# Performance work log

Measured on AMD Instinct MI355X. Metric: run time of the kernel, lower is better.

The kernel has to match this reference:

```python
import jax, jax.numpy as jnp
import numpy as np

HEADS = 16
MAX_SEQ_LEN = 1024
ALPHA = 1.0


def setup_inputs() -> dict:
    key = jax.random.key(0)
    ks = jax.random.split(key, 16)
    b, n, dim = 2, 1024, 1024
    s = 0.02
    x = jax.random.normal(ks[0], (b, n, dim), jnp.float32)
    Wq = jax.random.normal(ks[1], (dim, dim), jnp.float32) * s
    Wk = jax.random.normal(ks[2], (dim, dim), jnp.float32) * s
    Wv = jax.random.normal(ks[3], (dim, dim), jnp.float32) * s
    Wo = jax.random.normal(ks[4], (dim, dim), jnp.float32) * s
    E_idx = jax.random.normal(ks[5], (MAX_SEQ_LEN, HEADS), jnp.float32) * s
    # padding_idx=0 rows zero-initialized (as in torch nn.Embedding(padding_idx=0))
    E_bar = (jax.random.normal(ks[6], (17, HEADS), jnp.float32) * s).at[0].set(0.0)
    E_pos = (jax.random.normal(ks[7], (96, HEADS), jnp.float32) * s).at[0].set(0.0)
    E_oct = (jax.random.normal(ks[8], (25, HEADS), jnp.float32) * s).at[0].set(0.0)
    E_semi = (jax.random.normal(ks[9], (13, HEADS), jnp.float32) * s).at[0].set(0.0)
    # structure matrices: raw values in [0, table_size-2]; forward adds +1
    bar = jax.random.randint(ks[10], (b, n, n), 0, 16, dtype=jnp.int32)
    position = jax.random.randint(ks[11], (b, n, n), 0, 95, dtype=jnp.int32)
    octave = jax.random.randint(ks[12], (b, n, n), 0, 24, dtype=jnp.int32)
    semitone = jax.random.randint(ks[13], (b, n, n), 0, 12, dtype=jnp.int32)
    return {"x": x, "Wq": Wq, "Wk": Wk, "Wv": Wv, "Wo": Wo,
            "E_idx": E_idx, "E_bar": E_bar, "E_pos": E_pos,
            "E_oct": E_oct, "E_semi": E_semi,
            "bar": bar, "position": position, "octave": octave, "semitone": semitone}


def reference(x, Wq, Wk, Wv, Wo, E_idx, E_bar, E_pos, E_oct, E_semi,
              bar, position, octave, semitone):
    b, n, dim = x.shape
    h = HEADS
    d = dim // h

    def split_heads(t):  # (b,n,dim) -> (b,h,n,d)
        return t.reshape(b, n, h, d).transpose(0, 2, 1, 3)

    q = split_heads(x @ Wq.T)
    k = split_heads(x @ Wk.T)
    v = split_heads(x @ Wv.T)

    qk = jnp.einsum('bhid,bhjd->bhij', q, k)

    # relative index bias: (1,h,n,n)
    rel_pos = jnp.clip(jnp.arange(n)[:, None] - jnp.arange(n)[None, :], 0, MAX_SEQ_LEN - 1)
    srel = E_idx[rel_pos].transpose(2, 0, 1)[None]

    # structure biases: embedding lookups -> (b,h,n,n)
    s_time = (E_bar[bar + 1] + E_pos[position + 1]).transpose(0, 3, 1, 2)
    s_pitch = (E_oct[octave + 1] + E_semi[semitone + 1]).transpose(0, 3, 1, 2)

    dots = (qk + ALPHA * (srel + s_time + s_pitch)) / jnp.sqrt(jnp.float32(d))

    causal_mask = jnp.triu(jnp.ones((n, n), dtype=bool), k=1)
    mask_value = -jnp.finfo(dots.dtype).max
    dots = jnp.where(causal_mask, mask_value, dots)

    attn = jax.nn.softmax(dots, axis=-1)  # dropout=0 at eval
    out = jnp.einsum('bhij,bhjd->bhid', attn, v)
    out = out.transpose(0, 2, 1, 3).reshape(b, n, dim)
    return out @ Wo.T
```

## Files before the change

kernel.cpp:

```cpp
#include <hip/hip_runtime.h>
#include <cstdint>
#include <math.h>

typedef __attribute__((ext_vector_type(8))) short short8;
typedef __attribute__((ext_vector_type(4))) float f32x4;

#define LOG2E 1.44269504088896340736f

static __device__ __forceinline__ float bf2f(unsigned short u) {
    union { unsigned int i; float f; } v; v.i = ((unsigned int)u) << 16; return v.f;
}
static __device__ __forceinline__ unsigned short f2bf(float f) {
    union { float f; unsigned int i; } v; v.f = f;
    unsigned int r = v.i + 0x7FFF + ((v.i >> 16) & 1);
    return (unsigned short)(r >> 16);
}

__global__ __launch_bounds__(256) void k_prep(
    const float* __restrict__ x, const float* __restrict__ wq,
    const float* __restrict__ wk, const float* __restrict__ wv,
    const float* __restrict__ wo, unsigned short* __restrict__ dstconv,
    const float* __restrict__ Eidx, const float* __restrict__ Ebar,
    const float* __restrict__ Epos, const float* __restrict__ Eoct,
    const float* __restrict__ Esemi,
    const int* __restrict__ barm, const int* __restrict__ posm,
    const int* __restrict__ octm, const int* __restrict__ semim,
    unsigned short* __restrict__ biasg) {
    __shared__ float2 t2[8 * 233];
    __shared__ int    pk[16 * 65];

    if (blockIdx.x >= 1088) {
        long t = (long)(blockIdx.x - 1088) * 256 + threadIdx.x;
        long base = t * 4;
        const long NX = 2097152, NW = 1048576;
        const float* src; long off;
        if (base < NX)            { src = x;  off = base; }
        else if (base < NX + NW)  { src = wq; off = base - NX; }
        else if (base < NX + 2*NW){ src = wk; off = base - NX - NW; }
        else if (base < NX + 3*NW){ src = wv; off = base - NX - 2*NW; }
        else                      { src = wo; off = base - NX - 3*NW; }
        float4 v = *(const float4*)(src + off);
        ushort4 o;
        o.x = f2bf(v.x); o.y = f2bf(v.y); o.z = f2bf(v.z); o.w = f2bf(v.w);
        *(ushort4*)(dstconv + base) = o;
        return;
    }
    int fid = blockIdx.x;
    int b = (fid >= 544) ? 1 : 0;
    int f = fid - b * 544;
    int ti, tj;
    if (f >= 480) { int rr = f - 480; ti = 60 + (rr >> 4); tj = rr & 15; }
    else {
        int g = (int)(0.5f * (sqrtf(1.0f + 2.0f * (float)f) - 1.0f));
        while (2 * (g + 1) * (g + 2) <= f) g++;
        while (2 * g * (g + 1) > f) g--;
        int rr = f - 2 * g * (g + 1);
        int q = rr / (g + 1);
        ti = g * 4 + q;
        tj = rr - q * (g + 1);
    }
    int i0 = ti * 16, j0 = tj * 64;

    int t = threadIdx.x;
    int rel_lo = i0 - j0 - 63; if (rel_lo < 0) rel_lo = 0;

    for (int idx = t; idx < 231 * 8; idx += 256) {
        int s = idx >> 3, h2 = idx & 7;
        float va, vb;
        if (s < 80) {
            int src = rel_lo + s; if (src > 1023) src = 1023;
            va = Eidx[src * 16 + h2]; vb = Eidx[src * 16 + h2 + 8];
        } else if (s < 97)  { va = Ebar[(s - 80) * 16 + h2];  vb = Ebar[(s - 80) * 16 + h2 + 8]; }
        else if (s < 193)   { va = Epos[(s - 97) * 16 + h2];  vb = Epos[(s - 97) * 16 + h2 + 8]; }
        else if (s < 218)   { va = Eoct[(s - 193) * 16 + h2]; vb = Eoct[(s - 193) * 16 + h2 + 8]; }
        else                { va = Esemi[(s - 218) * 16 + h2]; vb = Esemi[(s - 218) * 16 + h2 + 8]; }
        t2[h2 * 233 + s] = make_float2(va, vb);
    }
    #pragma unroll
    for (int cc = 0; cc < 4; cc++) {
        int cell = t + cc * 256;
        int i = i0 + (cell >> 6), j = j0 + (cell & 63);
        long ij = ((long)b << 20) + ((long)i << 10) + j;
        int v = (barm[ij] + 1) | ((posm[ij] + 1) << 5) |
                ((octm[ij] + 1) << 12) | ((semim[ij] + 1) << 17);
        pk[(cell >> 6) * 65 + (cell & 63)] = v;
    }
    __syncthreads();

    int lane = t & 63, q = t & 15, G = (t >> 4) & 3, hq = t >> 6;
    int base_rel = (i0 + q) - j0 - rel_lo;
    const float2* TA = &t2[hq * 233];
    const float2* TB = &t2[(hq + 4) * 233];
    long tbase = ((((long)(b * 16) * 64 + ti) * 16 + tj) << 10) + lane * 16;
    #pragma unroll
    for (int sub = 0; sub < 4; sub++) {
        ushort4 o0, o1, o2, o3;
        #pragma unroll
        for (int rr = 0; rr < 4; rr++) {
            int key = sub * 16 + G * 4 + rr;
            int p = pk[q * 65 + key];
            int sr = base_rel - key; if (sr < 0) sr = 0;
            float2 a0 = TA[sr];
            float2 a1 = TA[80  + (p & 31)];
            float2 a2 = TA[97  + ((p >> 5)  & 127)];
            float2 a3 = TA[193 + ((p >> 12) & 31)];
            float2 a4 = TA[218 + ((p >> 17) & 15)];
            float2 b0 = TB[sr];
            float2 b1 = TB[80  + (p & 31)];
            float2 b2 = TB[97  + ((p >> 5)  & 127)];
            float2 b3 = TB[193 + ((p >> 12) & 31)];
            float2 b4 = TB[218 + ((p >> 17) & 15)];
            float xA = a0.x + a1.x + a2.x + a3.x + a4.x;
            float yA = a0.y + a1.y + a2.y + a3.y + a4.y;
            float xB = b0.x + b1.x + b2.x + b3.x + b4.x;
            float yB = b0.y + b1.y + b2.y + b3.y + b4.y;
            ((unsigned short*)&o0)[rr] = f2bf(xA * 0.125f);
            ((unsigned short*)&o1)[rr] = f2bf(xB * 0.125f);
            ((unsigned short*)&o2)[rr] = f2bf(yA * 0.125f);
            ((unsigned short*)&o3)[rr] = f2bf(yB * 0.125f);
        }
        *(ushort4*)(biasg + tbase + ((long)hq        << 20) + sub * 4) = o0;
        *(ushort4*)(biasg + tbase + ((long)(hq + 4)  << 20) + sub * 4) = o1;
        *(ushort4*)(biasg + tbase + ((long)(hq + 8)  << 20) + sub * 4) = o2;
        *(ushort4*)(biasg + tbase + ((long)(hq + 12) << 20) + sub * 4) = o3;
    }
}

__global__ __launch_bounds__(256) void k_gemm(
    const unsigned short* __restrict__ A,
    const unsigned short* __restrict__ B0, const unsigned short* __restrict__ B1,
    const unsigned short* __restrict__ B2,
    unsigned short* __restrict__ qd, unsigned short* __restrict__ kd,
    unsigned short* __restrict__ vtd, float* __restrict__ outf, int mode) {
    __shared__ unsigned short As[128 * 64];
    __shared__ unsigned short Bs[64 * 64];
    int md = (mode < 0) ? (int)blockIdx.z : mode;
    const unsigned short* B = (md == 1) ? B1 : (md == 2) ? B2 : B0;
    int m0 = blockIdx.x * 128, n0 = blockIdx.y * 64;
    int t = threadIdx.x;
    int w = t >> 6, lane = t & 63, g = lane >> 4, c = lane & 15;
    int wr = w >> 1, wc = w & 1;
    const int K = 1024;
    f32x4 zero = {0.f, 0.f, 0.f, 0.f};
    f32x4 acc[4][2];
    #pragma unroll
    for (int m = 0; m < 4; m++)
        #pragma unroll
        for (int n = 0; n < 2; n++) acc[m][n] = zero;

    int srow = w * 8 + (lane >> 3);
    int scol = (lane & 7) * 8;
    for (int k0 = 0; k0 < K; k0 += 64) {
        __syncthreads();
        #pragma unroll
        for (int qq = 0; qq < 4; qq++) {
            int row = qq * 32 + srow;
            __builtin_amdgcn_global_load_lds(
                (const __attribute__((address_space(1))) unsigned int*)(A + (long)(m0 + row) * K + k0 + scol),
                (__attribute__((address_space(3))) unsigned int*)&As[(qq * 32 + w * 8) * 64],
                16, 0, 0);
        }
        #pragma unroll
        for (int qq = 0; qq < 2; qq++) {
            int row = qq * 32 + srow;
            __builtin_amdgcn_global_load_lds(
                (const __attribute__((address_space(1))) unsigned int*)(B + (long)(n0 + row) * K + k0 + scol),
                (__attribute__((address_space(3))) unsigned int*)&Bs[(qq * 32 + w * 8) * 64],
                16, 0, 0);
        }
        __syncthreads();
        #pragma unroll
        for (int kk = 0; kk < 2; kk++) {
            short8 a[4], bb[2];
            #pragma unroll
            for (int m = 0; m < 4; m++)
                a[m] = *(const short8*)&As[(wr * 64 + m * 16 + c) * 64 + kk * 32 + g * 8];
            #pragma unroll
            for (int n = 0; n < 2; n++)
                bb[n] = *(const short8*)&Bs[(wc * 32 + n * 16 + c) * 64 + kk * 32 + g * 8];
            #pragma unroll
            for (int m = 0; m < 4; m++)
                #pragma unroll
                for (int n = 0; n < 2; n++)
                    acc[m][n] = __builtin_amdgcn_mfma_f32_16x16x32_bf16(a[m], bb[n], acc[m][n], 0, 0, 0);
        }
    }

    if (md <= 1) {
        unsigned short* dst = (md == 0) ? qd : kd;
        float scale = (md == 0) ? 0.125f : 1.0f;
        #pragma unroll
        for (int m = 0; m < 4; m++) {
            #pragma unroll
            for (int r = 0; r < 4; r++) {
                int mm = m0 + wr * 64 + m * 16 + g * 4 + r;
                int bb2 = mm >> 10, ii = mm & 1023;
                #pragma unroll
                for (int n = 0; n < 2; n++) {
                    int nn = n0 + wc * 32 + n * 16 + c;
                    int hh = nn >> 6, dd = nn & 63;
                    dst[(((long)(bb2 * 16 + hh) << 10) + ii) * 64 + dd] = f2bf(acc[m][n][r] * scale);
                }
            }
        }
    } else if (md == 2) {
        #pragma unroll
        for (int m = 0; m < 4; m++) {
            int mm0 = m0 + wr * 64 + m * 16 + g * 4;
            int bb2 = mm0 >> 10, ii = mm0 & 1023;
            #pragma unroll
            for (int n = 0; n < 2; n++) {
                int nn = n0 + wc * 32 + n * 16 + c;
                int hh = nn >> 6, dd = nn & 63;
                ushort4 pkv;
                pkv.x = f2bf(acc[m][n][0]); pkv.y = f2bf(acc[m][n][1]);
                pkv.z = f2bf(acc[m][n][2]); pkv.w = f2bf(acc[m][n][3]);
                *(ushort4*)&vtd[(((long)(bb2 * 16 + hh) << 6) + dd) * 1024 + ii] = pkv;
            }
        }
    } else {
        #pragma unroll
        for (int m = 0; m < 4; m++) {
            #pragma unroll
            for (int r = 0; r < 4; r++) {
                long mm = m0 + wr * 64 + m * 16 + g * 4 + r;
                #pragma unroll
                for (int n = 0; n < 2; n++) {
                    int nn = n0 + wc * 32 + n * 16 + c;
                    outf[mm * 1024 + nn] = acc[m][n][r];
                }
            }
        }
    }
}

#define LOADT(KA, KB, BV, JT) do {                                             \
    int _j0 = (JT) * 64;                                                       \
    _Pragma("unroll")                                                          \
    for (int _s = 0; _s < 4; _s++) {                                           \
        const unsigned short* _kr = Kp + (long)(_j0 + _s * 16 + c) * 64 + g * 8; \
        KA[_s] = *(const short8*)(_kr);                                        \
        KB[_s] = *(const short8*)(_kr + 32);                                   \
    }                                                                          \
    const unsigned short* _bp = Bt + ((JT) << 10) + lane * 16;                 \
    BV[0] = *(const short8*)(_bp);                                             \
    BV[1] = *(const short8*)(_bp + 8);                                         \
} while (0)

#define BODY(KA, KB, BV, JT) do {                                             \
    int _j0 = (JT) * 64;                                                      \
    f32x4 _s[4];                                                              \
    _Pragma("unroll")                                                         \
    for (int _sub = 0; _sub < 4; _sub++) {                                    \
        _s[_sub] = __builtin_amdgcn_mfma_f32_16x16x32_bf16(KA[_sub], q0, zero, 0, 0, 0); \
        _s[_sub] = __builtin_amdgcn_mfma_f32_16x16x32_bf16(KB[_sub], q1, _s[_sub], 0, 0, 0); \
    }                                                                         \
    short8 _v0[4], _v1[4];                                                    \
    _Pragma("unroll")                                                         \
    for (int _dd = 0; _dd < 4; _dd++) {                                       \
        const unsigned short* _vb = Vp + (long)(_dd * 16 + c) * 1024 + _j0 + g * 8; \
        _v0[_dd] = *(const short8*)(_vb);                                     \
        _v1[_dd] = *(const short8*)(_vb + 32);                                \
    }                                                                         \
    unsigned int _P0[4], _P1[4];                                              \
    _Pragma("unroll")                                                         \
    for (int _sub = 0; _sub < 4; _sub++) {                                    \
        float _pe[4];                                                         \
        _Pragma("unroll")                                                     \
        for (int _r = 0; _r < 4; _r++) {                                      \
            int _idx = _sub * 4 + _r;                                         \
            float _ss = _s[_sub][_r] +                                        \
                ((_idx < 8) ? bf2f((unsigned short)BV[0][_idx])               \
                            : bf2f((unsigned short)BV[1][_idx - 8]));         \
            if ((JT) == nj - 1 && _j0 + _sub * 16 + g * 4 + _r > i0 + c)      \
                _ss = -1e9f;                                                  \
            _pe[_r] = exp2f(__builtin_fmaf(_ss, LOG2E, -8.0f * LOG2E));       \
            l += _pe[_r];                                                     \
        }                                                                     \
        asm("v_cvt_pk_bf16_f32 %0, %1, %2" : "=v"(_P0[_sub]) : "v"(_pe[0]), "v"(_pe[1])); \
        asm("v_cvt_pk_bf16_f32 %0, %1, %2" : "=v"(_P1[_sub]) : "v"(_pe[2]), "v"(_pe[3])); \
    }                                                                         \
    _Pragma("unroll")                                                         \
    for (int _ch = 0; _ch < 2; _ch++) {                                       \
        unsigned int _a0 = (unsigned int)__shfl((int)_P0[_ch * 2],     srcA); \
        unsigned int _a1 = (unsigned int)__shfl((int)_P0[_ch * 2 + 1], srcA); \
        unsigned int _b0 = (unsigned int)__shfl((int)_P1[_ch * 2],     srcA); \
        unsigned int _b1 = (unsigned int)__shfl((int)_P1[_ch * 2 + 1], srcA); \
        unsigned int _c0 = (unsigned int)__shfl((int)_P0[_ch * 2],     srcB); \
        unsigned int _c1 = (unsigned int)__shfl((int)_P0[_ch * 2 + 1], srcB); \
        unsigned int _d0 = (unsigned int)__shfl((int)_P1[_ch * 2],     srcB); \
        unsigned int _d1 = (unsigned int)__shfl((int)_P1[_ch * 2 + 1], srcB); \
        union { unsigned int u[4]; short8 s8; } _pb;                          \
        _pb.u[0] = sel ? _a1 : _a0;                                           \
        _pb.u[1] = sel ? _b1 : _b0;                                           \
        _pb.u[2] = sel ? _c1 : _c0;                                           \
        _pb.u[3] = sel ? _d1 : _d0;                                           \
        _Pragma("unroll")                                                     \
        for (int _dd = 0; _dd < 4; _dd++)                                     \
            o[_dd] = __builtin_amdgcn_mfma_f32_16x16x32_bf16(                 \
                (_ch == 0) ? _v0[_dd] : _v1[_dd], _pb.s8, o[_dd], 0, 0, 0);   \
    }                                                                         \
} while (0)

__global__ __launch_bounds__(256) void k_attn(
    const unsigned short* __restrict__ Qs, const unsigned short* __restrict__ Ks,
    const unsigned short* __restrict__ VTs, const unsigned short* __restrict__ biasg,
    unsigned short* __restrict__ Os) {
    __shared__ char smem[4 * 4672];
    int bid = blockIdx.x;
    int it = 63 - (bid >> 5);
    int bh = bid & 31;
    int b = bh >> 4, h = bh & 15;
    int w = threadIdx.x >> 6;
    int lane = threadIdx.x & 63;
    int g = lane >> 4, c = lane & 15;
    int i0 = it * 16;
    int srcA = ((lane >> 4) & 1) * 32 + c;
    int srcB = srcA + 16;
    int sel  = (lane >> 5) & 1;

    char* wbase = smem + w * 4672;

    long plane = ((long)bh) << 16;
    const unsigned short* Qp = Qs + plane;
    const unsigned short* Kp = Ks + plane;
    const unsigned short* Vp = VTs + plane;
    const unsigned short* Bt = biasg + (((long)bh * 64 + it) << 14);

    short8 q0 = *(const short8*)(Qp + (long)(i0 + c) * 64 + g * 8);
    short8 q1 = *(const short8*)(Qp + (long)(i0 + c) * 64 + 32 + g * 8);

    f32x4 zero = {0.f, 0.f, 0.f, 0.f};
    f32x4 o[4]; o[0] = zero; o[1] = zero; o[2] = zero; o[3] = zero;
    float l = 0.f;

    int nj = (it >> 2) + 1;
    short8 kaA[4], kbA[4], bvA[2];
    short8 kaB[4], kbB[4], bvB[2];
    if (w < nj) LOADT(kaA, kbA, bvA, w);
    for (int jt = w; jt < nj; jt += 8) {
        if (jt + 4 < nj) LOADT(kaB, kbB, bvB, jt + 4);
        BODY(kaA, kbA, bvA, jt);
        if (jt + 4 < nj) {
            if (jt + 8 < nj) LOADT(kaA, kbA, bvA, jt + 8);
            BODY(kaB, kbB, bvB, jt + 4);
        }
    }
    float* oc = (float*)wbase;
    float* lc = (float*)(wbase + 4352);
    #pragma unroll
    for (int db = 0; db < 4; db++)
        #pragma unroll
        for (int r = 0; r < 4; r++)
            oc[lane * 17 + db * 4 + r] = o[db][r];
    lc[lane] = l;
    __syncthreads();

    {
        int db = w;
        float lv = 0.f;
        #pragma unroll
        for (int ww = 0; ww < 4; ww++)
            lv += ((const float*)(smem + ww * 4672 + 4352))[lane];
        lv += __shfl_xor(lv, 16);
        lv += __shfl_xor(lv, 32);
        float linv = 1.0f / lv;
        float ov[4];
        #pragma unroll
        for (int r = 0; r < 4; r++) {
            float s = 0.f;
            #pragma unroll
            for (int ww = 0; ww < 4; ww++)
                s += ((const float*)(smem + ww * 4672))[lane * 17 + db * 4 + r];
            ov[r] = s;
        }
        int i = i0 + c;
        unsigned short* op = Os + ((long)(b * 1024 + i)) * 1024 + h * 64 + db * 16 + g * 4;
        ushort4 o4;
        o4.x = f2bf(ov[0] * linv); o4.y = f2bf(ov[1] * linv);
        o4.z = f2bf(ov[2] * linv); o4.w = f2bf(ov[3] * linv);
        *(ushort4*)op = o4;
    }
}

extern "C" void kernel_launch(void* const* d_in, const int* in_sizes, int n_in,
                              void* d_out, int out_size, void* d_ws, size_t ws_size,
                              hipStream_t stream) {
    const float* x     = (const float*)d_in[0];
    const float* Wq    = (const float*)d_in[1];
    const float* Wk    = (const float*)d_in[2];
    const float* Wv    = (const float*)d_in[3];
    const float* Wo    = (const float*)d_in[4];
    const float* Eidx  = (const float*)d_in[5];
    const float* Ebar  = (const float*)d_in[6];
    const float* Epos  = (const float*)d_in[7];
    const float* Eoct  = (const float*)d_in[8];
    const float* Esemi = (const float*)d_in[9];
    const int* barm    = (const int*)d_in[10];
    const int* posm    = (const int*)d_in[11];
    const int* octm    = (const int*)d_in[12];
    const int* semim   = (const int*)d_in[13];
    float* outf = (float*)d_out;

    unsigned short* w = (unsigned short*)d_ws;
    unsigned short* XB   = w;
    unsigned short* WQB  = w + 2097152;
    unsigned short* WKB  = w + 3145728;
    unsigned short* WVB  = w + 4194304;
    unsigned short* WOB  = w + 5242880;
    unsigned short* QS   = w + 6291456;
    unsigned short* KS   = w + 8388608;
    unsigned short* VTS  = w + 10485760;
    unsigned short* OS   = w + 12582912;
    unsigned short* BIAS = w + 14680064;

    k_prep<<<7232, 256, 0, stream>>>(x, Wq, Wk, Wv, Wo, w,
                                     Eidx, Ebar, Epos, Eoct, Esemi,
                                     barm, posm, octm, semim, BIAS);
    k_gemm<<<dim3(16, 16, 3), 256, 0, stream>>>(XB, WQB, WKB, WVB,
                                                QS, KS, VTS, nullptr, -1);
    k_attn<<<2048, 256, 0, stream>>>(QS, KS, VTS, BIAS, OS);
    k_gemm<<<dim3(16, 16, 1), 256, 0, stream>>>(OS, WOB, WOB, WOB,
                                                QS, KS, VTS, outf, 3);
}
```

Baseline: 103.5 us.

## Assign one query tile per wave instead of splitting KV across waves

The attention kernel previously had four waves share one 16-row query tile, splitting the KV tiles among them and reducing partial outputs through shared memory with a block barrier. Now each wave owns its own query tile (four consecutive tiles per block), walks all KV tiles sequentially, and writes its output directly, which removes the LDS reduction and the sync. The grid shrinks to 512 blocks with a reordered tile mapping for load balance. The cost is longer serial KV loops per wave and fewer blocks, which may reduce parallelism and latency hiding on the causal triangle.

```diff
diff --git a/kernel.cpp b/kernel.cpp
--- a/kernel.cpp
+++ b/kernel.cpp
@@ -306,20 +306,18 @@
     const unsigned short* __restrict__ Qs, const unsigned short* __restrict__ Ks,
     const unsigned short* __restrict__ VTs, const unsigned short* __restrict__ biasg,
     unsigned short* __restrict__ Os) {
-    __shared__ char smem[4 * 4672];
     int bid = blockIdx.x;
-    int it = 63 - (bid >> 5);
+    int itg = (bid < 256) ? (15 - (bid >> 5)) : ((bid - 256) >> 5);
     int bh = bid & 31;
     int b = bh >> 4, h = bh & 15;
     int w = threadIdx.x >> 6;
     int lane = threadIdx.x & 63;
     int g = lane >> 4, c = lane & 15;
+    int it = itg * 4 + w;
     int i0 = it * 16;
     int srcA = ((lane >> 4) & 1) * 32 + c;
     int srcB = srcA + 16;
     int sel  = (lane >> 5) & 1;
-
-    char* wbase = smem + w * 4672;
 
     long plane = ((long)bh) << 16;
     const unsigned short* Qp = Qs + plane;
@@ -334,52 +332,30 @@
     f32x4 o[4]; o[0] = zero; o[1] = zero; o[2] = zero; o[3] = zero;
     float l = 0.f;
 
-    int nj = (it >> 2) + 1;
+    int nj = itg + 1;
     short8 kaA[4], kbA[4], bvA[2];
     short8 kaB[4], kbB[4], bvB[2];
-    if (w < nj) LOADT(kaA, kbA, bvA, w);
-    for (int jt = w; jt < nj; jt += 8) {
-        if (jt + 4 < nj) LOADT(kaB, kbB, bvB, jt + 4);
+    LOADT(kaA, kbA, bvA, 0);
+    for (int jt = 0; jt < nj; jt += 2) {
+        if (jt + 1 < nj) LOADT(kaB, kbB, bvB, jt + 1);
         BODY(kaA, kbA, bvA, jt);
-        if (jt + 4 < nj) {
-            if (jt + 8 < nj) LOADT(kaA, kbA, bvA, jt + 8);
-            BODY(kaB, kbB, bvB, jt + 4);
-        }
-    }
-    float* oc = (float*)wbase;
-    float* lc = (float*)(wbase + 4352);
+        if (jt + 1 < nj) {
+            if (jt + 2 < nj) LOADT(kaA, kbA, bvA, jt + 2);
+            BODY(kaB, kbB, bvB, jt + 1);
+        }
+    }
+    float lv = l;
+    lv += __shfl_xor(lv, 16);
+    lv += __shfl_xor(lv, 32);
+    float linv = 1.0f / lv;
+    int i = i0 + c;
+    unsigned short* op = Os + ((long)(b * 1024 + i)) * 1024 + h * 64 + g * 4;
     #pragma unroll
-    for (int db = 0; db < 4; db++)
-        #pragma unroll
-        for (int r = 0; r < 4; r++)
-            oc[lane * 17 + db * 4 + r] = o[db][r];
-    lc[lane] = l;
-    __syncthreads();
-
-    {
-        int db = w;
-        float lv = 0.f;
-        #pragma unroll
-        for (int ww = 0; ww < 4; ww++)
-            lv += ((const float*)(smem + ww * 4672 + 4352))[lane];
-        lv += __shfl_xor(lv, 16);
-        lv += __shfl_xor(lv, 32);
-        float linv = 1.0f / lv;
-        float ov[4];
-        #pragma unroll
-        for (int r = 0; r < 4; r++) {
-            float s = 0.f;
-            #pragma unroll
-            for (int ww = 0; ww < 4; ww++)
-                s += ((const float*)(smem + ww * 4672))[lane * 17 + db * 4 + r];
-            ov[r] = s;
-        }
-        int i = i0 + c;
-        unsigned short* op = Os + ((long)(b * 1024 + i)) * 1024 + h * 64 + db * 16 + g * 4;
+    for (int db = 0; db < 4; db++) {
         ushort4 o4;
-        o4.x = f2bf(ov[0] * linv); o4.y = f2bf(ov[1] * linv);
-        o4.z = f2bf(ov[2] * linv); o4.w = f2bf(ov[3] * linv);
-        *(ushort4*)op = o4;
+        o4.x = f2bf(o[db][0] * linv); o4.y = f2bf(o[db][1] * linv);
+        o4.z = f2bf(o[db][2] * linv); o4.w = f2bf(o[db][3] * linv);
+        *(ushort4*)(op + db * 16) = o4;
     }
 }
 
@@ -419,7 +395,7 @@
                                      barm, posm, octm, semim, BIAS);
     k_gemm<<<dim3(16, 16, 3), 256, 0, stream>>>(XB, WQB, WKB, WVB,
                                                 QS, KS, VTS, nullptr, -1);
-    k_attn<<<2048, 256, 0, stream>>>(QS, KS, VTS, BIAS, OS);
+    k_attn<<<512, 256, 0, stream>>>(QS, KS, VTS, BIAS, OS);
     k_gemm<<<dim3(16, 16, 1), 256, 0, stream>>>(OS, WOB, WOB, WOB,
                                                 QS, KS, VTS, outf, 3);
 }
```

After: 100.5 us, median of 3. -2.9%, faster.
